# Optimization experiments

Hardware: AMD Instinct MI355X
Metric: run time of the kernel (lower is better)

Reference implementation:

```python
import jax, jax.numpy as jnp
import numpy as np

G, T, S, M = 128, 512, 24, 4


def setup_inputs() -> dict:
    key = jax.random.key(0)
    k0, k1, k2, k3, k4 = jax.random.split(key, 5)
    inp = jax.random.normal(k0, (G, T, M), dtype=jnp.float32)
    # Stable-ish transition matrices: near 0.95*I
    F = 0.95 * jnp.eye(S, dtype=jnp.float32) + 0.05 * jax.random.normal(k1, (G, T, S, S), dtype=jnp.float32) / jnp.sqrt(S)
    # PSD process noise Q = c*A A^T + eps*I
    Aq = jax.random.normal(k2, (G, T, S, S), dtype=jnp.float32)
    Q = (0.01 / S) * jnp.einsum('gtik,gtjk->gtij', Aq, Aq) + 1e-3 * jnp.eye(S, dtype=jnp.float32)
    H = 0.5 * jax.random.normal(k3, (G, T, M, S), dtype=jnp.float32)
    # PSD measurement noise R
    Ar = jax.random.normal(k4, (G, T, M, M), dtype=jnp.float32)
    R = (0.1 / M) * jnp.einsum('gtik,gtjk->gtij', Ar, Ar) + 1e-2 * jnp.eye(M, dtype=jnp.float32)
    init_mean = jnp.zeros((G, S), dtype=jnp.float32)
    init_cov = jnp.broadcast_to(jnp.eye(S, dtype=jnp.float32), (G, S, S))
    return dict(input=inp, F=F, Q=Q, H=H, R=R, init_mean=init_mean, init_cov=init_cov)


def _measure(m, P, Hc, Rc):
    # one-step-ahead measurement distribution: mu = H m, Sig = H P H^T + R
    mu = jnp.einsum('gms,gs->gm', Hc, m)
    Sig = Hc @ P @ Hc.swapaxes(-1, -2) + Rc
    return mu, Sig


def _kalman(input, F, Q, H, R, init_mean, init_cov):
    # time-major for scan
    y = jnp.moveaxis(input, 1, 0)      # [T,G,M]
    Ft = jnp.moveaxis(F, 1, 0)         # [T,G,S,S]
    Qt = jnp.moveaxis(Q, 1, 0)
    Ht = jnp.moveaxis(H, 1, 0)         # [T,G,M,S]
    Rt = jnp.moveaxis(R, 1, 0)         # [T,G,M,M]

    mu0, Sig0 = _measure(init_mean, init_cov, Ht[0], Rt[0])

    def step(carry, x):
        m, P = carry                     # state prediction for t-1: [G,S], [G,S,S]
        yprev, Fp, Qp, Hp, Rp, Hc, Rc = x
        # --- update with obs at t-1 (using H,R from the t-1 measurement) ---
        HP = Hp @ P                      # [G,M,S]
        Sm = HP @ Hp.swapaxes(-1, -2) + Rp   # innovation cov [G,M,M]
        # K = P H^T S^{-1}; using symmetry: K = solve(S, H P)^T
        K = jnp.linalg.solve(Sm, HP).swapaxes(-1, -2)  # [G,S,M]
        resid = yprev - jnp.einsum('gms,gs->gm', Hp, m)
        m_u = m + jnp.einsum('gsm,gm->gs', K, resid)
        P_u = P - K @ HP
        # --- predict to t ---
        m_p = jnp.einsum('gij,gj->gi', Fp, m_u)
        P_p = Fp @ P_u @ Fp.swapaxes(-1, -2) + Qp
        # --- measurement at t ---
        mu, Sig = _measure(m_p, P_p, Hc, Rc)
        return (m_p, P_p), (mu, Sig)

    xs = (y[:-1], Ft[:-1], Qt[:-1], Ht[:-1], Rt[:-1], Ht[1:], Rt[1:])
    _, (mus, Sigs) = jax.lax.scan(step, (init_mean, init_cov), xs)
    means = jnp.moveaxis(jnp.concatenate([mu0[None], mus], axis=0), 0, 1)   # [G,T,M]
    covs = jnp.moveaxis(jnp.concatenate([Sig0[None], Sigs], axis=0), 0, 1)  # [G,T,M,M]
    return means, covs


def reference(input, F, Q, H, R, init_mean, init_cov):
    return _kalman(input, F, Q, H, R, init_mean, init_cov)
```

## Files before the change

### kernel.cpp

```cpp
#include <hip/hip_runtime.h>

#define Gn 128
#define Tn 512
#define Sn 24
#define SP 28
#define Mn 4
#define COVS_BASE (Gn * Tn * Mn)

__device__ __forceinline__ float4 ld4(const float* p) {
    return *reinterpret_cast<const float4*>(p);
}
__device__ __forceinline__ void st4(float* p, float4 v) {
    *reinterpret_cast<float4*>(p) = v;
}
__device__ __forceinline__ float dot4(float4 a, float4 b) {
    return a.x*b.x + a.y*b.y + a.z*b.z + a.w*b.w;
}

struct Row24 { float4 v[6]; };

__device__ __forceinline__ Row24 loadRow(const float* p) {
    Row24 r;
#pragma unroll
    for (int i = 0; i < 6; ++i) r.v[i] = ld4(p + 4*i);
    return r;
}

__device__ __forceinline__ float dot24(const Row24& a, const float* b) {
    float4 b0 = ld4(b+0), b1 = ld4(b+4), b2 = ld4(b+8),
           b3 = ld4(b+12), b4 = ld4(b+16), b5 = ld4(b+20);
    float s0 = a.v[0].x*b0.x + a.v[0].y*b0.y + a.v[0].z*b0.z + a.v[0].w*b0.w;
    float s1 = a.v[1].x*b1.x + a.v[1].y*b1.y + a.v[1].z*b1.z + a.v[1].w*b1.w;
    float s2 = a.v[2].x*b2.x + a.v[2].y*b2.y + a.v[2].z*b2.z + a.v[2].w*b2.w;
    float s3 = a.v[3].x*b3.x + a.v[3].y*b3.y + a.v[3].z*b3.z + a.v[3].w*b3.w;
    float s4 = a.v[4].x*b4.x + a.v[4].y*b4.y + a.v[4].z*b4.z + a.v[4].w*b4.w;
    float s5 = a.v[5].x*b5.x + a.v[5].y*b5.y + a.v[5].z*b5.z + a.v[5].w*b5.w;
    return ((s0+s1)+(s2+s3))+(s4+s5);
}

__device__ __forceinline__ void barrierLds() {
    asm volatile("s_waitcnt lgkmcnt(0)" ::: "memory");
    __builtin_amdgcn_s_barrier();
    asm volatile("" ::: "memory");
}
__device__ __forceinline__ void waveLds() {
    asm volatile("s_waitcnt lgkmcnt(0)" ::: "memory");
    __builtin_amdgcn_wave_barrier();
    asm volatile("" ::: "memory");
}

extern "C" __global__ void __launch_bounds__(256)
kalman_kernel(const float* __restrict__ y_g, const float* __restrict__ F_g,
              const float* __restrict__ Q_g, const float* __restrict__ H_g,
              const float* __restrict__ R_g, const float* __restrict__ m0_g,
              const float* __restrict__ P0_g, float* __restrict__ out)
{
    const int g   = blockIdx.x;
    const int tid = threadIdx.x;
    const int gT  = g * Tn;

    __shared__ __align__(16) float sP[Sn*SP];
    __shared__ __align__(16) float sG[Sn*SP];
    __shared__ __align__(16) float sF[2][Sn*SP];
    __shared__ __align__(16) float sQ[2][Sn*SP];
    __shared__ __align__(16) float sH[2][Mn*SP];
    __shared__ __align__(16) float sR[2][16];
    __shared__ __align__(16) float sy[2][4];
    __shared__ __align__(16) float sHP[Mn*SP];
    __shared__ __align__(16) float sV[Sn*4];
    __shared__ __align__(16) float sSm[16];
    __shared__ __align__(16) float sInv[16];
    __shared__ __align__(16) float sMean[Sn];
    __shared__ __align__(16) float sFm[Sn];
    __shared__ __align__(16) float sResid[4];
    __shared__ __align__(16) float sr2[4];

    const float4* F4 = reinterpret_cast<const float4*>(F_g);
    const float4* Q4 = reinterpret_cast<const float4*>(Q_g);
    const float4* H4 = reinterpret_cast<const float4*>(H_g);
    const float4* R4 = reinterpret_cast<const float4*>(R_g);
    const float4* y4 = reinterpret_cast<const float4*>(y_g);

    auto stage_load = [&](int v, int t) -> float4 {
        if (v < 144)      return F4[(gT + t)*144 + v];
        else if (v < 288) return Q4[(gT + t)*144 + (v-144)];
        else if (v < 312) return H4[(gT + t)*24  + (v-288)];
        else if (v < 316) return R4[(gT + t)*4   + (v-312)];
        else              return y4[gT + t];
    };
    auto stage_store = [&](int v, int bb, float4 val) {
        if (v < 144)      { int r = v/6,        c = (v%6)*4;           st4(&sF[bb][r*SP+c], val); }
        else if (v < 288) { int v2 = v-144; int r = v2/6, c = (v2%6)*4; st4(&sQ[bb][r*SP+c], val); }
        else if (v < 312) { int v2 = v-288; int r = v2/6, c = (v2%6)*4; st4(&sH[bb][r*SP+c], val); }
        else if (v < 316) { st4(&sR[bb][(v-312)*4], val); }
        else              { st4(&sy[bb][0], val); }
    };

    if (tid < 144) {
        int r = tid / 6, c = (tid % 6) * 4;
        st4(&sP[r*SP + c], ld4(&P0_g[g*Sn*Sn + tid*4]));
    } else if (tid < 150) {
        int v = tid - 144;
        st4(&sMean[v*4], ld4(&m0_g[g*Sn + v*4]));
    }
    {
        float4 a0 = stage_load(tid, 0);
        stage_store(tid, 0, a0);
        if (tid < 61) {
            float4 a1 = stage_load(tid + 256, 0);
            stage_store(tid + 256, 0, a1);
        }
    }
    barrierLds();

    float4 pf0, pf1;

    for (int t = 0; t < Tn; ++t) {
        const int  b    = t & 1;
        const int  b1   = b ^ 1;
        const bool last = (t == Tn - 1);

        if (!last) {
            pf0 = stage_load(tid, t+1);
            if (tid < 61) pf1 = stage_load(tid + 256, t+1);
        }
        if (tid < 96) {
            int a = tid / 24, s = tid % 24;
            Row24 hr = loadRow(&sH[b][a*SP]);
            sHP[a*SP + s] = dot24(hr, &sP[s*SP]);
        } else if (tid < 100) {
            int a = tid - 96;
            Row24 hr = loadRow(&sH[b][a*SP]);
            float mu = dot24(hr, sMean);
            out[(gT + t)*4 + a] = mu;
            sResid[a] = sy[b][a] - mu;
        } else if (!last) {
            int o0 = 3*(tid - 100);
            int i = o0/24, j0 = o0%24;
            Row24 fr = loadRow(&sF[b][i*SP]);
#pragma unroll
            for (int d = 0; d < 3; ++d) {
                sG[i*SP + j0 + d] = dot24(fr, &sP[(j0+d)*SP]);
            }
        }
        barrierLds();

        if (tid < 64) {
            if (!last) {
                if (tid < 32) {
                    int v0 = 3*tid;
                    int a = v0/24, i0 = v0%24;
                    Row24 hpr = loadRow(&sHP[a*SP]);
#pragma unroll
                    for (int d = 0; d < 3; ++d) {
                        int i = i0 + d;
                        sV[i*4 + a] = dot24(hpr, &sF[b][i*SP]);
                    }
                } else if (tid < 40) {
                    int i0 = 3*(tid - 32);
#pragma unroll
                    for (int d = 0; d < 3; ++d) {
                        int i = i0 + d;
                        Row24 fr = loadRow(&sF[b][i*SP]);
                        sFm[i] = dot24(fr, sMean);
                    }
                } else {
                    int o0 = 468 + 3*(tid - 40);
                    int i = o0/24, j0 = o0%24;
                    Row24 fr = loadRow(&sF[b][i*SP]);
#pragma unroll
                    for (int d = 0; d < 3; ++d) {
                        sG[i*SP + j0 + d] = dot24(fr, &sP[(j0+d)*SP]);
                    }
                }
            }
        } else if (tid < 128) {
            if (!last && tid < 76) {
                int o0 = 540 + 3*(tid - 64);
                int i = o0/24, j0 = o0%24;
                Row24 fr = loadRow(&sF[b][i*SP]);
#pragma unroll
                for (int d = 0; d < 3; ++d) {
                    sG[i*SP + j0 + d] = dot24(fr, &sP[(j0+d)*SP]);
                }
            }
        } else if (tid < 192) {
            if (tid < 144) {
                int idx = tid - 128;
                int a = idx >> 2, c = idx & 3;
                Row24 hpr = loadRow(&sHP[a*SP]);
                float sig = dot24(hpr, &sH[b][c*SP]) + sR[b][idx];
                sSm[idx] = sig;
                out[COVS_BASE + (size_t)(gT + t)*16 + idx] = sig;
            }
            if (!last) {
                waveLds();
                if (tid < 144) {
                    int idx = tid - 128;
                    float s00=sSm[0],  s01=sSm[1],  s02=sSm[2],  s03=sSm[3];
                    float s10=sSm[4],  s11=sSm[5],  s12=sSm[6],  s13=sSm[7];
                    float s20=sSm[8],  s21=sSm[9],  s22=sSm[10], s23=sSm[11];
                    float s30=sSm[12], s31=sSm[13], s32=sSm[14], s33=sSm[15];
                    float p0 = s00*s11 - s01*s10;
                    float p1 = s00*s12 - s02*s10;
                    float p2 = s00*s13 - s03*s10;
                    float p3 = s01*s12 - s02*s11;
                    float p4 = s01*s13 - s03*s11;
                    float p5 = s02*s13 - s03*s12;
                    float q0c = s20*s31 - s21*s30;
                    float q1c = s20*s32 - s22*s30;
                    float q2c = s20*s33 - s23*s30;
                    float q3c = s21*s32 - s22*s31;
                    float q4c = s21*s33 - s23*s31;
                    float q5c = s22*s33 - s23*s32;
                    float det  = p0*q5c - p1*q4c + p2*q3c + p3*q2c - p4*q1c + p5*q0c;
                    float rdet = 1.0f / det;
                    int ia = idx >> 2, ic = idx & 3;
                    int r0 = (ic==0)?1:0, r1 = (ic<=1)?2:1, r2i = (ic<=2)?3:2;
                    int u0 = (ia==0)?1:0, u1 = (ia<=1)?2:1, u2 = (ia<=2)?3:2;
                    float m00=sSm[r0*4+u0], m01=sSm[r0*4+u1], m02=sSm[r0*4+u2];
                    float m10=sSm[r1*4+u0], m11=sSm[r1*4+u1], m12=sSm[r1*4+u2];
                    float m20=sSm[r2i*4+u0], m21=sSm[r2i*4+u1], m22=sSm[r2i*4+u2];
                    float minor = m00*(m11*m22 - m12*m21)
                                - m01*(m10*m22 - m12*m20)
                                + m02*(m10*m21 - m11*m20);
                    float cof = ((ia + ic) & 1) ? -minor : minor;
                    sInv[idx] = cof * rdet;
                }
                waveLds();
                if (tid < 132) {
                    int a = tid - 128;
                    sr2[a] = dot4(ld4(&sInv[a*4]), ld4(&sResid[0]));
                }
            }
        }
        if (last) return;
        barrierLds();

        if (tid < 192) {
            int o0 = 3*tid;
            int i = o0/24, j0 = o0%24;
            Row24 gr = loadRow(&sG[i*SP]);
            float4 vi   = ld4(&sV[i*4]);
            float4 inv0 = ld4(&sInv[0]),  inv1 = ld4(&sInv[4]);
            float4 inv2 = ld4(&sInv[8]),  inv3 = ld4(&sInv[12]);
#pragma unroll
            for (int d = 0; d < 3; ++d) {
                int j = j0 + d;
                float4 vj = ld4(&sV[j*4]);
                float4 tj;
                tj.x = dot4(inv0, vj);
                tj.y = dot4(inv1, vj);
                tj.z = dot4(inv2, vj);
                tj.w = dot4(inv3, vj);
                float val = dot24(gr, &sF[b][j*SP]) + sQ[b][i*SP + j] - dot4(vi, tj);
                sP[i*SP + j] = val;
            }
        } else if (tid < 216) {
            int s = tid - 192;
            sMean[s] = sFm[s] + dot4(ld4(&sV[s*4]), ld4(&sr2[0]));
        }
        stage_store(tid, b1, pf0);
        if (tid < 61) stage_store(tid + 256, b1, pf1);
        barrierLds();
    }
}

extern "C" void kernel_launch(void* const* d_in, const int* in_sizes, int n_in,
                              void* d_out, int out_size, void* d_ws, size_t ws_size,
                              hipStream_t stream) {
    kalman_kernel<<<Gn, 256, 0, stream>>>(
        (const float*)d_in[0], (const float*)d_in[1], (const float*)d_in[2],
        (const float*)d_in[3], (const float*)d_in[4], (const float*)d_in[5],
        (const float*)d_in[6], (float*)d_out);
}
```

Baseline: 1.571 ms.

## Remap thread work so FPᵀ product is split across phases with stationary rows

Reassigns per-thread work by wave and lane so that each lane keeps one row of F or H in registers and sweeps columns of P, producing G = F·P and H·P together in phase one. The F·P·Fᵀ product moves into phase two, held in registers (part[]), running alongside the innovation inverse on wave 3. Phase three then only adds Q and the rank-4 correction. The aim is a better balance of the three barrier-separated phases and fewer redundant LDS row loads. The cost is more branching inside each wave and more live registers.

```diff
diff --git a/kernel.cpp b/kernel.cpp
--- a/kernel.cpp
+++ b/kernel.cpp
@@ -55,9 +55,13 @@
               const float* __restrict__ R_g, const float* __restrict__ m0_g,
               const float* __restrict__ P0_g, float* __restrict__ out)
 {
-    const int g   = blockIdx.x;
-    const int tid = threadIdx.x;
-    const int gT  = g * Tn;
+    const int g    = blockIdx.x;
+    const int tid  = threadIdx.x;
+    const int gT   = g * Tn;
+    const int lane = tid & 63;
+    const int w    = tid >> 6;
+    const int h    = lane >> 5;
+    const int r    = lane & 31;
 
     __shared__ __align__(16) float sP[Sn*SP];
     __shared__ __align__(16) float sG[Sn*SP];
@@ -89,16 +93,16 @@
         else              return y4[gT + t];
     };
     auto stage_store = [&](int v, int bb, float4 val) {
-        if (v < 144)      { int r = v/6,        c = (v%6)*4;           st4(&sF[bb][r*SP+c], val); }
-        else if (v < 288) { int v2 = v-144; int r = v2/6, c = (v2%6)*4; st4(&sQ[bb][r*SP+c], val); }
-        else if (v < 312) { int v2 = v-288; int r = v2/6, c = (v2%6)*4; st4(&sH[bb][r*SP+c], val); }
+        if (v < 144)      { int rr = v/6,        c = (v%6)*4;            st4(&sF[bb][rr*SP+c], val); }
+        else if (v < 288) { int v2 = v-144; int rr = v2/6, c = (v2%6)*4; st4(&sQ[bb][rr*SP+c], val); }
+        else if (v < 312) { int v2 = v-288; int rr = v2/6, c = (v2%6)*4; st4(&sH[bb][rr*SP+c], val); }
         else if (v < 316) { st4(&sR[bb][(v-312)*4], val); }
         else              { st4(&sy[bb][0], val); }
     };
 
     if (tid < 144) {
-        int r = tid / 6, c = (tid % 6) * 4;
-        st4(&sP[r*SP + c], ld4(&P0_g[g*Sn*Sn + tid*4]));
+        int rr = tid / 6, c = (tid % 6) * 4;
+        st4(&sP[rr*SP + c], ld4(&P0_g[g*Sn*Sn + tid*4]));
     } else if (tid < 150) {
         int v = tid - 144;
         st4(&sMean[v*4], ld4(&m0_g[g*Sn + v*4]));
@@ -114,6 +118,7 @@
     barrierLds();
 
     float4 pf0, pf1;
+    float  part[4];
 
     for (int t = 0; t < Tn; ++t) {
         const int  b    = t & 1;
@@ -124,79 +129,39 @@
             pf0 = stage_load(tid, t+1);
             if (tid < 61) pf1 = stage_load(tid + 256, t+1);
         }
-        if (tid < 96) {
-            int a = tid / 24, s = tid % 24;
-            Row24 hr = loadRow(&sH[b][a*SP]);
-            sHP[a*SP + s] = dot24(hr, &sP[s*SP]);
-        } else if (tid < 100) {
-            int a = tid - 96;
-            Row24 hr = loadRow(&sH[b][a*SP]);
-            float mu = dot24(hr, sMean);
-            out[(gT + t)*4 + a] = mu;
-            sResid[a] = sy[b][a] - mu;
-        } else if (!last) {
-            int o0 = 3*(tid - 100);
-            int i = o0/24, j0 = o0%24;
-            Row24 fr = loadRow(&sF[b][i*SP]);
+        {
+            const float* statp = (r < 24) ? &sF[b][r*SP]
+                                          : &sH[b][((r-24)&3)*SP];
+            Row24 stat = loadRow(statp);
 #pragma unroll
             for (int d = 0; d < 3; ++d) {
-                sG[i*SP + j0 + d] = dot24(fr, &sP[(j0+d)*SP]);
+                int j = 6*w + 3*h + d;
+                const float* bp = (r < 28) ? &sP[j*SP] : &sMean[0];
+                float val = dot24(stat, bp);
+                if (r < 24) {
+                    sG[r*SP + j] = val;
+                } else if (r < 28) {
+                    sHP[(r-24)*SP + j] = val;
+                } else if (d == 0 && h == 0 && w == 0) {
+                    int a = r - 28;
+                    out[(gT + t)*4 + a] = val;
+                    sResid[a] = sy[b][a] - val;
+                }
             }
         }
         barrierLds();
 
-        if (tid < 64) {
-            if (!last) {
-                if (tid < 32) {
-                    int v0 = 3*tid;
-                    int a = v0/24, i0 = v0%24;
-                    Row24 hpr = loadRow(&sHP[a*SP]);
-#pragma unroll
-                    for (int d = 0; d < 3; ++d) {
-                        int i = i0 + d;
-                        sV[i*4 + a] = dot24(hpr, &sF[b][i*SP]);
-                    }
-                } else if (tid < 40) {
-                    int i0 = 3*(tid - 32);
-#pragma unroll
-                    for (int d = 0; d < 3; ++d) {
-                        int i = i0 + d;
-                        Row24 fr = loadRow(&sF[b][i*SP]);
-                        sFm[i] = dot24(fr, sMean);
-                    }
-                } else {
-                    int o0 = 468 + 3*(tid - 40);
-                    int i = o0/24, j0 = o0%24;
-                    Row24 fr = loadRow(&sF[b][i*SP]);
-#pragma unroll
-                    for (int d = 0; d < 3; ++d) {
-                        sG[i*SP + j0 + d] = dot24(fr, &sP[(j0+d)*SP]);
-                    }
-                }
-            }
-        } else if (tid < 128) {
-            if (!last && tid < 76) {
-                int o0 = 540 + 3*(tid - 64);
-                int i = o0/24, j0 = o0%24;
-                Row24 fr = loadRow(&sF[b][i*SP]);
-#pragma unroll
-                for (int d = 0; d < 3; ++d) {
-                    sG[i*SP + j0 + d] = dot24(fr, &sP[(j0+d)*SP]);
-                }
-            }
-        } else if (tid < 192) {
-            if (tid < 144) {
-                int idx = tid - 128;
-                int a = idx >> 2, c = idx & 3;
+        if (w == 3) {
+            if (lane < 16) {
+                int a = lane >> 2, c = lane & 3;
                 Row24 hpr = loadRow(&sHP[a*SP]);
-                float sig = dot24(hpr, &sH[b][c*SP]) + sR[b][idx];
-                sSm[idx] = sig;
-                out[COVS_BASE + (size_t)(gT + t)*16 + idx] = sig;
+                float sig = dot24(hpr, &sH[b][c*SP]) + sR[b][lane];
+                sSm[lane] = sig;
+                out[COVS_BASE + (size_t)(gT + t)*16 + lane] = sig;
             }
             if (!last) {
                 waveLds();
-                if (tid < 144) {
-                    int idx = tid - 128;
+                if (lane < 16) {
                     float s00=sSm[0],  s01=sSm[1],  s02=sSm[2],  s03=sSm[3];
                     float s10=sSm[4],  s11=sSm[5],  s12=sSm[6],  s13=sSm[7];
                     float s20=sSm[8],  s21=sSm[9],  s22=sSm[10], s23=sSm[11];
@@ -215,50 +180,70 @@
                     float q5c = s22*s33 - s23*s32;
                     float det  = p0*q5c - p1*q4c + p2*q3c + p3*q2c - p4*q1c + p5*q0c;
                     float rdet = 1.0f / det;
-                    int ia = idx >> 2, ic = idx & 3;
+                    int ia = lane >> 2, ic = lane & 3;
                     int r0 = (ic==0)?1:0, r1 = (ic<=1)?2:1, r2i = (ic<=2)?3:2;
                     int u0 = (ia==0)?1:0, u1 = (ia<=1)?2:1, u2 = (ia<=2)?3:2;
-                    float m00=sSm[r0*4+u0], m01=sSm[r0*4+u1], m02=sSm[r0*4+u2];
-                    float m10=sSm[r1*4+u0], m11=sSm[r1*4+u1], m12=sSm[r1*4+u2];
+                    float m00=sSm[r0*4+u0],  m01=sSm[r0*4+u1],  m02=sSm[r0*4+u2];
+                    float m10=sSm[r1*4+u0],  m11=sSm[r1*4+u1],  m12=sSm[r1*4+u2];
                     float m20=sSm[r2i*4+u0], m21=sSm[r2i*4+u1], m22=sSm[r2i*4+u2];
                     float minor = m00*(m11*m22 - m12*m21)
                                 - m01*(m10*m22 - m12*m20)
                                 + m02*(m10*m21 - m11*m20);
                     float cof = ((ia + ic) & 1) ? -minor : minor;
-                    sInv[idx] = cof * rdet;
+                    sInv[lane] = cof * rdet;
                 }
                 waveLds();
-                if (tid < 132) {
-                    int a = tid - 128;
-                    sr2[a] = dot4(ld4(&sInv[a*4]), ld4(&sResid[0]));
+                if (lane < 4) {
+                    sr2[lane] = dot4(ld4(&sInv[lane*4]), ld4(&sResid[0]));
+                }
+            }
+        } else if (!last) {
+            if (r < 24) {
+                Row24 gr = loadRow(&sG[r*SP]);
+#pragma unroll
+                for (int d = 0; d < 4; ++d) {
+                    int j = 8*w + 4*h + d;
+                    part[d] = dot24(gr, &sF[b][j*SP]);
+                }
+            } else {
+                int q = w*16 + h*8 + (r - 24);
+                if (q < 32) {
+                    int a = q >> 3, i0 = (q & 7) * 3;
+                    Row24 hpr = loadRow(&sHP[a*SP]);
+#pragma unroll
+                    for (int d = 0; d < 3; ++d)
+                        sV[(i0+d)*4 + a] = dot24(hpr, &sF[b][(i0+d)*SP]);
+                } else if (q < 40) {
+                    int i0 = (q - 32) * 3;
+                    Row24 mr = loadRow(&sMean[0]);
+#pragma unroll
+                    for (int d = 0; d < 3; ++d)
+                        sFm[i0+d] = dot24(mr, &sF[b][(i0+d)*SP]);
                 }
             }
         }
         if (last) return;
         barrierLds();
 
-        if (tid < 192) {
-            int o0 = 3*tid;
-            int i = o0/24, j0 = o0%24;
-            Row24 gr = loadRow(&sG[i*SP]);
-            float4 vi   = ld4(&sV[i*4]);
-            float4 inv0 = ld4(&sInv[0]),  inv1 = ld4(&sInv[4]);
-            float4 inv2 = ld4(&sInv[8]),  inv3 = ld4(&sInv[12]);
-#pragma unroll
-            for (int d = 0; d < 3; ++d) {
-                int j = j0 + d;
-                float4 vj = ld4(&sV[j*4]);
-                float4 tj;
-                tj.x = dot4(inv0, vj);
-                tj.y = dot4(inv1, vj);
-                tj.z = dot4(inv2, vj);
-                tj.w = dot4(inv3, vj);
-                float val = dot24(gr, &sF[b][j*SP]) + sQ[b][i*SP + j] - dot4(vi, tj);
-                sP[i*SP + j] = val;
-            }
-        } else if (tid < 216) {
-            int s = tid - 192;
-            sMean[s] = sFm[s] + dot4(ld4(&sV[s*4]), ld4(&sr2[0]));
+        if (w < 3) {
+            if (r < 24) {
+                float4 vr  = ld4(&sV[r*4]);
+                float4 i0v = ld4(&sInv[0]),  i1v = ld4(&sInv[4]);
+                float4 i2v = ld4(&sInv[8]),  i3v = ld4(&sInv[12]);
+                float4 ur;
+                ur.x = dot4(i0v, vr); ur.y = dot4(i1v, vr);
+                ur.z = dot4(i2v, vr); ur.w = dot4(i3v, vr);
+#pragma unroll
+                for (int d = 0; d < 4; ++d) {
+                    int j = 8*w + 4*h + d;
+                    float4 vj = ld4(&sV[j*4]);
+                    sP[r*SP + j] = part[d] + sQ[b][r*SP + j] - dot4(ur, vj);
+                }
+            }
+        } else {
+            if (lane < 24) {
+                sMean[lane] = sFm[lane] + dot4(ld4(&sV[lane*4]), ld4(&sr2[0]));
+            }
         }
         stage_store(tid, b1, pf0);
         if (tid < 61) stage_store(tid + 256, b1, pf1);
```

Measured after the change: 1.292 ms. -17.8%, faster.
